# Kernel tuning notes

Measured on AMD Instinct MI355X. Metric: run time of the kernel, lower is better.

The kernel has to match this reference:

```python
import jax, jax.numpy as jnp
import numpy as np

N = 100000
E = 1600000
IN_FEATS = 128
H_FEATS = 128
NUM_CLASSES = 64
BN_EPS = 1e-5


def setup_inputs() -> dict:
    key = jax.random.key(0)
    ks = jax.random.split(key, 16)
    inp = {
        "in_feat": jax.random.normal(ks[0], (N, IN_FEATS), dtype=jnp.float32),
        "src": jax.random.randint(ks[1], (E,), 0, N, dtype=jnp.int64),
        "dst": jax.random.randint(ks[2], (E,), 0, N, dtype=jnp.int64),
        # GraphConv weights (glorot-ish scale) and biases
        "W0": jax.random.normal(ks[3], (IN_FEATS, H_FEATS), dtype=jnp.float32) / np.sqrt(IN_FEATS),
        "b0": jnp.zeros((H_FEATS,), dtype=jnp.float32),
        "W1": jax.random.normal(ks[4], (H_FEATS, H_FEATS), dtype=jnp.float32) / np.sqrt(H_FEATS),
        "b1": jnp.zeros((H_FEATS,), dtype=jnp.float32),
        "W2": jax.random.normal(ks[5], (H_FEATS, NUM_CLASSES), dtype=jnp.float32) / np.sqrt(H_FEATS),
        "b2": jnp.zeros((NUM_CLASSES,), dtype=jnp.float32),
        # BatchNorm affine params
        "gamma0": jnp.ones((H_FEATS,), dtype=jnp.float32),
        "beta0": jnp.zeros((H_FEATS,), dtype=jnp.float32),
        "gamma1": jnp.ones((H_FEATS,), dtype=jnp.float32),
        "beta1": jnp.zeros((H_FEATS,), dtype=jnp.float32),
    }
    return inp


def _graph_conv(src, dst, h, W, b):
    # DGL GraphConv, norm='both': D_dst^{-1/2} A (D_src^{-1/2} h W) + b
    ones = jnp.ones((src.shape[0],), dtype=h.dtype)
    deg_out = jnp.clip(jax.ops.segment_sum(ones, src, num_segments=N), 1.0)
    deg_in = jnp.clip(jax.ops.segment_sum(ones, dst, num_segments=N), 1.0)
    h = h * jax.lax.rsqrt(deg_out)[:, None]
    h = h @ W  # mult weight before aggregation (same math either way)
    agg = jax.ops.segment_sum(h[src], dst, num_segments=N)  # SpMM
    return agg * jax.lax.rsqrt(deg_in)[:, None] + b


def _batch_norm(h, gamma, beta):
    # BatchNorm1d in training mode: biased batch stats over the node axis
    mean = jnp.mean(h, axis=0)
    var = jnp.mean(jnp.square(h - mean), axis=0)
    return (h - mean) * jax.lax.rsqrt(var + BN_EPS) * gamma + beta


def reference(in_feat, src, dst, W0, b0, W1, b1, W2, b2, gamma0, beta0, gamma1, beta1):
    h = _graph_conv(src, dst, in_feat, W0, b0)
    h = jax.nn.relu(_batch_norm(h, gamma0, beta0))  # dropout p=0 -> identity
    h = _graph_conv(src, dst, h, W1, b1)
    h = jax.nn.relu(_batch_norm(h, gamma1, beta1))
    return _graph_conv(src, dst, h, W2, b2)
```

## Files before the change

kernel.cpp:

```cpp
#include <hip/hip_runtime.h>

#define NFEAT 128
#define BT 2048
#define BSH 9
#define BSZ 512
#define NP 256

typedef __attribute__((ext_vector_type(8))) short short8v;
typedef __attribute__((ext_vector_type(4))) float float4v;

static inline size_t align_up(size_t x, size_t a) { return (x + a - 1) & ~(a - 1); }

__device__ inline unsigned short f2bf(float f) {
  unsigned u = __float_as_uint(f);
  u += 0x7FFF + ((u >> 16) & 1);
  return (unsigned short)(u >> 16);
}
__device__ inline unsigned pack2bf(float lo, float hi) {
  return ((unsigned)f2bf(lo)) | (((unsigned)f2bf(hi)) << 16);
}
__device__ inline float bflo(unsigned u) { return __uint_as_float(u << 16); }
__device__ inline float bfhi(unsigned u) { return __uint_as_float(u & 0xFFFF0000u); }

__global__ __launch_bounds__(256) void k_bcount(const int* __restrict__ src,
                                                const int* __restrict__ dst,
                                                int* __restrict__ cnt, int E, int nb, int NBK) {
  __shared__ int hD[256], hS[256];
  const int t = threadIdx.x, b = blockIdx.x;
  hD[t] = 0; hS[t] = 0;
  __syncthreads();
  const int e0 = b * BT, e1 = min(E, e0 + BT);
  for (int e = e0 + t; e < e1; e += 256) {
    atomicAdd(&hD[dst[e] >> BSH], 1);
    atomicAdd(&hS[src[e] >> BSH], 1);
  }
  __syncthreads();
  if (t < NBK) {
    cnt[t * nb + b] = hD[t];
    cnt[(NBK + t) * nb + b] = hS[t];
  }
}

__global__ __launch_bounds__(512) void k_scanA(const int* __restrict__ in,
                                               int* __restrict__ out,
                                               int* __restrict__ bsum, int n) {
  __shared__ int tmp[512];
  const int t = threadIdx.x;
  const int i = blockIdx.x * 512 + t;
  int v = (i < n) ? in[i] : 0;
  tmp[t] = v;
  __syncthreads();
  for (int off = 1; off < 512; off <<= 1) {
    int y = (t >= off) ? tmp[t - off] : 0;
    __syncthreads();
    tmp[t] += y;
    __syncthreads();
  }
  int incl = tmp[t];
  if (i < n) out[i] = incl - v;
  if (t == 511) bsum[blockIdx.x] = incl;
}

__global__ __launch_bounds__(1024) void k_scanB(const int* __restrict__ bsum,
                                                int* __restrict__ bscan, int nb1) {
  __shared__ int tmp[1024];
  const int t = threadIdx.x;
  int v = (t < nb1) ? bsum[t] : 0;
  tmp[t] = v;
  __syncthreads();
  for (int off = 1; off < 1024; off <<= 1) {
    int y = (t >= off) ? tmp[t - off] : 0;
    __syncthreads();
    tmp[t] += y;
    __syncthreads();
  }
  bscan[t] = tmp[t] - v;
}

__global__ __launch_bounds__(512) void k_scanC(int* __restrict__ out,
                                               const int* __restrict__ bscan, int n) {
  const int i = blockIdx.x * 512 + threadIdx.x;
  if (i < n) out[i] += bscan[blockIdx.x];
}

__global__ __launch_bounds__(256) void k_bplace(const int* __restrict__ src,
                                                const int* __restrict__ dst,
                                                const int* __restrict__ off,
                                                int* __restrict__ buf, int E, int nb, int NBK) {
  __shared__ int cD[256], cS[256];
  const int t = threadIdx.x, b = blockIdx.x;
  if (t < NBK) {
    cD[t] = off[t * nb + b];
    cS[t] = off[(NBK + t) * nb + b];
  }
  __syncthreads();
  const int e0 = b * BT, e1 = min(E, e0 + BT);
  for (int e = e0 + t; e < e1; e += 256) {
    int s = src[e];
    int d = dst[e];
    int pD = atomicAdd(&cD[d >> BSH], 1);
    buf[pD] = ((d & (BSZ - 1)) << 17) | s;
    int pS = atomicAdd(&cS[s >> BSH], 1);
    buf[pS] = s;
  }
}

__global__ __launch_bounds__(256) void k_bcsr(const int* __restrict__ buf,
                                              const int* __restrict__ off,
                                              int* __restrict__ row_ptr,
                                              float* __restrict__ rsq_in,
                                              int* __restrict__ col,
                                              int E, int nb, int NBK, int N) {
  const int k = blockIdx.x, t = threadIdx.x;
  const int lo = off[k * nb];
  const int hi = (k + 1 < NBK) ? off[(k + 1) * nb] : E;
  __shared__ int cnt[BSZ];
  __shared__ int sc[BSZ];
  __shared__ int part[64];
  cnt[t] = 0; cnt[t + 256] = 0;
  __syncthreads();
  for (int e = lo + t; e < hi; e += 256) atomicAdd(&cnt[((unsigned)buf[e]) >> 17], 1);
  __syncthreads();
  if (t < 64) {
    int r = 0;
#pragma unroll
    for (int j = 0; j < 8; ++j) r += cnt[t * 8 + j];
    part[t] = r;
  }
  __syncthreads();
  if (t == 0) {
    int run = 0;
    for (int i = 0; i < 64; ++i) { int v = part[i]; part[i] = run; run += v; }
  }
  __syncthreads();
  if (t < 64) {
    int run = part[t];
#pragma unroll
    for (int j = 0; j < 8; ++j) { int v = cnt[t * 8 + j]; sc[t * 8 + j] = run; run += v; }
  }
  __syncthreads();
  for (int idx = t; idx < BSZ; idx += 256) {
    int n = (k << BSH) + idx;
    if (n < N) {
      row_ptr[n] = lo + sc[idx];
      int c = cnt[idx]; if (c < 1) c = 1;
      rsq_in[n] = 1.0f / sqrtf((float)c);
    }
    cnt[idx] = sc[idx];
  }
  if (k == NBK - 1 && t == 0) row_ptr[N] = E;
  __syncthreads();
  for (int e = lo + t; e < hi; e += 256) {
    int w = buf[e];
    int p = atomicAdd(&cnt[((unsigned)w) >> 17], 1);
    col[lo + p] = w & 0x1FFFF;
  }
}

__global__ __launch_bounds__(256) void k_bdeg(const int* __restrict__ buf,
                                              const int* __restrict__ off,
                                              float* __restrict__ rsq_out,
                                              int E, int nb, int NBK, int N) {
  const int k = blockIdx.x, t = threadIdx.x;
  const int lo = off[(NBK + k) * nb];
  const int hi = (k + 1 < NBK) ? off[(NBK + k + 1) * nb] : 2 * E;
  __shared__ int cnt[BSZ];
  cnt[t] = 0; cnt[t + 256] = 0;
  __syncthreads();
  for (int e = lo + t; e < hi; e += 256) atomicAdd(&cnt[buf[e] & (BSZ - 1)], 1);
  __syncthreads();
  for (int idx = t; idx < BSZ; idx += 256) {
    int n = (k << BSH) + idx;
    if (n < N) {
      int c = cnt[idx]; if (c < 1) c = 1;
      rsq_out[n] = 1.0f / sqrtf((float)c);
    }
  }
}

__global__ __launch_bounds__(256) void k_wprep(const float* __restrict__ W0,
                                               const float* __restrict__ W1,
                                               const float* __restrict__ W2,
                                               unsigned short* __restrict__ Wt0,
                                               unsigned short* __restrict__ Wt1,
                                               unsigned short* __restrict__ Wt2) {
  int t = blockIdx.x * 256 + threadIdx.x;
  if (t < 16384) {
    int c = t >> 7, k = t & 127;
    Wt0[c * 128 + k] = f2bf(W0[k * 128 + c]);
  } else if (t < 32768) {
    int u = t - 16384;
    int c = u >> 7, k = u & 127;
    Wt1[c * 128 + k] = f2bf(W1[k * 128 + c]);
  } else if (t < 40960) {
    int u = t - 32768;
    int c = u >> 7, k = u & 127;
    Wt2[c * 128 + k] = f2bf(W2[k * 64 + c]);
  }
}

template <int CC>
__global__ __launch_bounds__(256) void k_gemm_mfma(
    const float* __restrict__ X32, const unsigned short* __restrict__ Xbf,
    const unsigned short* __restrict__ Wt,
    unsigned short* __restrict__ Ybf, const float* __restrict__ rsq_out,
    const float* __restrict__ bnscale, const float* __restrict__ bnshift,
    int Nrows, int mode) {
  constexpr int XBYTES = 64 * 256;
  constexpr int WBYTES = CC * 256;
  __shared__ __align__(16) char lds[XBYTES + WBYTES];
  const int tid = threadIdx.x;
  const int rowBase = blockIdx.x * 64;

  for (int u = tid; u < CC * 16; u += 256) {
    int c = u >> 4, kq = u & 15;
    uint4 v = *(const uint4*)(Wt + c * 128 + kq * 8);
    int byte = (c * 256 + kq * 16) ^ ((c & 7) << 4);
    *(uint4*)(&lds[XBYTES + byte]) = v;
  }
  if (mode == 0) {
#pragma unroll
    for (int i = 0; i < 8; ++i) {
      int u = tid + i * 256;
      int r = u >> 5, kq = u & 31;
      int gr = rowBase + r;
      float4 v = make_float4(0.f, 0.f, 0.f, 0.f);
      if (gr < Nrows) v = *(const float4*)(X32 + (size_t)gr * 128 + kq * 4);
      ushort4 o;
      o.x = f2bf(v.x); o.y = f2bf(v.y); o.z = f2bf(v.z); o.w = f2bf(v.w);
      int byte = (r * 256 + kq * 8) ^ ((r & 7) << 4);
      *(ushort4*)(&lds[byte]) = o;
    }
  } else {
#pragma unroll
    for (int i = 0; i < 4; ++i) {
      int u = tid + i * 256;
      int r = u >> 4, kq = u & 15;
      int gr = rowBase + r;
      uint4 v = make_uint4(0, 0, 0, 0);
      if (gr < Nrows) v = *(const uint4*)(Xbf + (size_t)gr * 128 + kq * 8);
      float f0 = bflo(v.x), f1 = bfhi(v.x), f2 = bflo(v.y), f3 = bfhi(v.y);
      float f4 = bflo(v.z), f5 = bfhi(v.z), f6 = bflo(v.w), f7 = bfhi(v.w);
      const float4 sA = *(const float4*)(bnscale + kq * 8);
      const float4 sB = *(const float4*)(bnscale + kq * 8 + 4);
      const float4 hA = *(const float4*)(bnshift + kq * 8);
      const float4 hB = *(const float4*)(bnshift + kq * 8 + 4);
      f0 = fmaxf(f0 * sA.x + hA.x, 0.f); f1 = fmaxf(f1 * sA.y + hA.y, 0.f);
      f2 = fmaxf(f2 * sA.z + hA.z, 0.f); f3 = fmaxf(f3 * sA.w + hA.w, 0.f);
      f4 = fmaxf(f4 * sB.x + hB.x, 0.f); f5 = fmaxf(f5 * sB.y + hB.y, 0.f);
      f6 = fmaxf(f6 * sB.z + hB.z, 0.f); f7 = fmaxf(f7 * sB.w + hB.w, 0.f);
      uint4 o;
      o.x = pack2bf(f0, f1); o.y = pack2bf(f2, f3);
      o.z = pack2bf(f4, f5); o.w = pack2bf(f6, f7);
      int byte = (r * 256 + kq * 16) ^ ((r & 7) << 4);
      *(uint4*)(&lds[byte]) = o;
    }
  }
  __syncthreads();

  const int wv = tid >> 6;
  const int l = tid & 63;
  const int l16 = l & 15, lk = l >> 4;

  short8v a[4];
  const int arow = wv * 16 + l16;
#pragma unroll
  for (int kk = 0; kk < 4; ++kk) {
    int byte = (arow * 256 + kk * 64 + lk * 16) ^ ((arow & 7) << 4);
    a[kk] = *(const short8v*)(&lds[byte]);
  }

  float4v acc[CC / 16];
#pragma unroll
  for (int ct = 0; ct < CC / 16; ++ct) acc[ct] = (float4v){0.f, 0.f, 0.f, 0.f};

#pragma unroll
  for (int ct = 0; ct < CC / 16; ++ct) {
    const int col = ct * 16 + l16;
#pragma unroll
    for (int kk = 0; kk < 4; ++kk) {
      int byte = XBYTES + ((col * 256 + kk * 64 + lk * 16) ^ ((col & 7) << 4));
      short8v b = *(const short8v*)(&lds[byte]);
      acc[ct] = __builtin_amdgcn_mfma_f32_16x16x32_bf16(a[kk], b, acc[ct], 0, 0, 0);
    }
  }

  const int row0 = rowBase + wv * 16 + lk * 4;
  float scr[4];
#pragma unroll
  for (int r = 0; r < 4; ++r) scr[r] = (row0 + r < Nrows) ? rsq_out[row0 + r] : 0.f;
#pragma unroll
  for (int ct = 0; ct < CC / 16; ++ct) {
#pragma unroll
    for (int r = 0; r < 4; ++r) {
      int row = row0 + r;
      if (row < Nrows)
        Ybf[(size_t)row * CC + ct * 16 + l16] = f2bf(acc[ct][r] * scr[r]);
    }
  }
}

template <int F, int OUT_BF>
__global__ __launch_bounds__(256) void k_spmm2(const int* __restrict__ row_ptr,
                                               const int* __restrict__ colidx,
                                               const unsigned short* __restrict__ xW,
                                               void* __restrict__ outv,
                                               const float* __restrict__ rsq_in,
                                               const float* __restrict__ bias, int Nrows) {
  constexpr int FL = F / 8;
  constexpr int G = 64 / FL;
  const int node = blockIdx.x * 4 + (threadIdx.x >> 6);
  if (node >= Nrows) return;
  const int l = threadIdx.x & 63;
  const int fl = l % FL, g = l / FL;
  const int e0 = row_ptr[node];
  const int e1 = row_ptr[node + 1];
  float acc[8] = {};
  int e = e0 + g;
  for (; e + G < e1; e += 2 * G) {
    int s0 = colidx[e];
    int s1 = colidx[e + G];
    uint4 v0 = *(const uint4*)&xW[(size_t)s0 * F + fl * 8];
    uint4 v1 = *(const uint4*)&xW[(size_t)s1 * F + fl * 8];
    acc[0] += bflo(v0.x); acc[1] += bfhi(v0.x); acc[2] += bflo(v0.y); acc[3] += bfhi(v0.y);
    acc[4] += bflo(v0.z); acc[5] += bfhi(v0.z); acc[6] += bflo(v0.w); acc[7] += bfhi(v0.w);
    acc[0] += bflo(v1.x); acc[1] += bfhi(v1.x); acc[2] += bflo(v1.y); acc[3] += bfhi(v1.y);
    acc[4] += bflo(v1.z); acc[5] += bfhi(v1.z); acc[6] += bflo(v1.w); acc[7] += bfhi(v1.w);
  }
  if (e < e1) {
    int s0 = colidx[e];
    uint4 v0 = *(const uint4*)&xW[(size_t)s0 * F + fl * 8];
    acc[0] += bflo(v0.x); acc[1] += bfhi(v0.x); acc[2] += bflo(v0.y); acc[3] += bfhi(v0.y);
    acc[4] += bflo(v0.z); acc[5] += bfhi(v0.z); acc[6] += bflo(v0.w); acc[7] += bfhi(v0.w);
  }
#pragma unroll
  for (int m = FL; m < 64; m <<= 1) {
#pragma unroll
    for (int j = 0; j < 8; ++j) acc[j] += __shfl_xor(acc[j], m);
  }
  if (g != 0) return;
  const float sc = rsq_in[node];
  const float4 bA = *(const float4*)&bias[fl * 8];
  const float4 bB = *(const float4*)&bias[fl * 8 + 4];
  float o0 = acc[0] * sc + bA.x, o1 = acc[1] * sc + bA.y;
  float o2 = acc[2] * sc + bA.z, o3 = acc[3] * sc + bA.w;
  float o4 = acc[4] * sc + bB.x, o5 = acc[5] * sc + bB.y;
  float o6 = acc[6] * sc + bB.z, o7 = acc[7] * sc + bB.w;
  if (OUT_BF) {
    uint4 w;
    w.x = pack2bf(o0, o1); w.y = pack2bf(o2, o3);
    w.z = pack2bf(o4, o5); w.w = pack2bf(o6, o7);
    *(uint4*)&((unsigned short*)outv)[(size_t)node * F + fl * 8] = w;
  } else {
    float* out = (float*)outv;
    *(float4*)&out[(size_t)node * F + fl * 8] = make_float4(o0, o1, o2, o3);
    *(float4*)&out[(size_t)node * F + fl * 8 + 4] = make_float4(o4, o5, o6, o7);
  }
}

__global__ __launch_bounds__(256) void k_bn_stats_bf(const unsigned short* __restrict__ h,
                                                     float* __restrict__ psum,
                                                     float* __restrict__ pssq, int Nrows) {
  const int t = threadIdx.x;
  const int fs = t & 15;
  const int rg = t >> 4;
  float s[8] = {}, ss[8] = {};
  for (int r = blockIdx.x * 16 + rg; r < Nrows; r += gridDim.x * 16) {
    uint4 v = *(const uint4*)&h[(size_t)r * 128 + fs * 8];
    float f0 = bflo(v.x), f1 = bfhi(v.x), f2 = bflo(v.y), f3 = bfhi(v.y);
    float f4 = bflo(v.z), f5 = bfhi(v.z), f6 = bflo(v.w), f7 = bfhi(v.w);
    s[0] += f0; ss[0] += f0 * f0; s[1] += f1; ss[1] += f1 * f1;
    s[2] += f2; ss[2] += f2 * f2; s[3] += f3; ss[3] += f3 * f3;
    s[4] += f4; ss[4] += f4 * f4; s[5] += f5; ss[5] += f5 * f5;
    s[6] += f6; ss[6] += f6 * f6; s[7] += f7; ss[7] += f7 * f7;
  }
#pragma unroll
  for (int m = 16; m < 64; m <<= 1) {
#pragma unroll
    for (int j = 0; j < 8; ++j) { s[j] += __shfl_xor(s[j], m); ss[j] += __shfl_xor(ss[j], m); }
  }
  __shared__ float lsum[4][128], lssq[4][128];
  const int wv = t >> 6, wl = t & 63;
  if (wl < 16) {
#pragma unroll
    for (int j = 0; j < 8; ++j) { lsum[wv][wl * 8 + j] = s[j]; lssq[wv][wl * 8 + j] = ss[j]; }
  }
  __syncthreads();
  if (t < 128) {
    psum[(size_t)blockIdx.x * 128 + t] = lsum[0][t] + lsum[1][t] + lsum[2][t] + lsum[3][t];
    pssq[(size_t)blockIdx.x * 128 + t] = lssq[0][t] + lssq[1][t] + lssq[2][t] + lssq[3][t];
  }
}

__global__ __launch_bounds__(256) void k_bn_final(const float* __restrict__ psum,
                                                  const float* __restrict__ pssq,
                                                  const float* __restrict__ gamma,
                                                  const float* __restrict__ beta,
                                                  float* __restrict__ scale,
                                                  float* __restrict__ shift, int Nrows) {
  const int t = threadIdx.x;
  const int f = t & 127, half = t >> 7;
  float s = 0.f, ss = 0.f;
  for (int b = half * (NP / 2); b < (half + 1) * (NP / 2); ++b) {
    s += psum[(size_t)b * 128 + f];
    ss += pssq[(size_t)b * 128 + f];
  }
  __shared__ float ls[2][128], lss[2][128];
  ls[half][f] = s; lss[half][f] = ss;
  __syncthreads();
  if (t < 128) {
    float sum = ls[0][t] + ls[1][t];
    float sumsq = lss[0][t] + lss[1][t];
    float inv_n = 1.0f / (float)Nrows;
    float mean = sum * inv_n;
    float var = sumsq * inv_n - mean * mean;
    if (var < 0.f) var = 0.f;
    float sc = gamma[t] * (1.0f / sqrtf(var + 1e-5f));
    scale[t] = sc;
    shift[t] = beta[t] - mean * sc;
  }
}

extern "C" void kernel_launch(void* const* d_in, const int* in_sizes, int n_in,
                              void* d_out, int out_size, void* d_ws, size_t ws_size,
                              hipStream_t stream) {
  const float* in_feat = (const float*)d_in[0];
  const int* src = (const int*)d_in[1];
  const int* dst = (const int*)d_in[2];
  const float* W0 = (const float*)d_in[3];
  const float* b0 = (const float*)d_in[4];
  const float* W1 = (const float*)d_in[5];
  const float* b1 = (const float*)d_in[6];
  const float* W2 = (const float*)d_in[7];
  const float* b2 = (const float*)d_in[8];
  const float* gamma0 = (const float*)d_in[9];
  const float* beta0 = (const float*)d_in[10];
  const float* gamma1 = (const float*)d_in[11];
  const float* beta1 = (const float*)d_in[12];
  float* out = (float*)d_out;

  const int N = in_sizes[0] / NFEAT;
  const int E = in_sizes[1];

  const int nb = (E + BT - 1) / BT;
  const int NBK = (N + BSZ - 1) / BSZ;
  const int L = 2 * NBK * nb;
  const int nb1 = (L + 511) / 512;

  char* p = (char*)d_ws;
  auto carve = [&](size_t bytes) {
    char* q = p;
    p += align_up(bytes, 256);
    return q;
  };
  int* cnt = (int*)carve((size_t)L * 4);
  int* off = (int*)carve((size_t)L * 4);
  int* bsum = (int*)carve(1024 * 4);
  int* bscan = (int*)carve(1024 * 4);
  int* row_ptr = (int*)carve((size_t)(N + 1) * 4);
  int* col = (int*)carve((size_t)E * 4);
  float* rsq_out = (float*)carve((size_t)N * 4);
  float* rsq_in = (float*)carve((size_t)N * 4);
  float* psum0 = (float*)carve((size_t)NP * 128 * 4);
  float* pssq0 = (float*)carve((size_t)NP * 128 * 4);
  float* psum1 = (float*)carve((size_t)NP * 128 * 4);
  float* pssq1 = (float*)carve((size_t)NP * 128 * 4);
  float* bn_scale0 = (float*)carve(128 * 4);
  float* bn_shift0 = (float*)carve(128 * 4);
  float* bn_scale1 = (float*)carve(128 * 4);
  float* bn_shift1 = (float*)carve(128 * 4);
  unsigned short* Wt0 = (unsigned short*)carve(16384 * 2);
  unsigned short* Wt1 = (unsigned short*)carve(16384 * 2);
  unsigned short* Wt2 = (unsigned short*)carve(8192 * 2);
  unsigned short* xWbf = (unsigned short*)carve((size_t)N * NFEAT * 2);
  unsigned short* hbf = (unsigned short*)carve((size_t)N * NFEAT * 2);
  int* buf = (int*)carve((size_t)2 * E * 4);

  k_wprep<<<160, 256, 0, stream>>>(W0, W1, W2, Wt0, Wt1, Wt2);
  k_bcount<<<nb, 256, 0, stream>>>(src, dst, cnt, E, nb, NBK);
  k_scanA<<<nb1, 512, 0, stream>>>(cnt, off, bsum, L);
  k_scanB<<<1, 1024, 0, stream>>>(bsum, bscan, nb1);
  k_scanC<<<nb1, 512, 0, stream>>>(off, bscan, L);
  k_bplace<<<nb, 256, 0, stream>>>(src, dst, off, buf, E, nb, NBK);
  k_bcsr<<<NBK, 256, 0, stream>>>(buf, off, row_ptr, rsq_in, col, E, nb, NBK, N);
  k_bdeg<<<NBK, 256, 0, stream>>>(buf, off, rsq_out, E, nb, NBK, N);

  const int GR = (N + 63) / 64;
  const int GS = (N + 3) / 4;

  k_gemm_mfma<128><<<GR, 256, 0, stream>>>(in_feat, nullptr, Wt0, xWbf, rsq_out,
                                           nullptr, nullptr, N, 0);
  k_spmm2<128, 1><<<GS, 256, 0, stream>>>(row_ptr, col, xWbf, hbf, rsq_in, b0, N);
  k_bn_stats_bf<<<NP, 256, 0, stream>>>(hbf, psum0, pssq0, N);
  k_bn_final<<<1, 256, 0, stream>>>(psum0, pssq0, gamma0, beta0, bn_scale0, bn_shift0, N);

  k_gemm_mfma<128><<<GR, 256, 0, stream>>>(nullptr, hbf, Wt1, xWbf, rsq_out,
                                           bn_scale0, bn_shift0, N, 1);
  k_spmm2<128, 1><<<GS, 256, 0, stream>>>(row_ptr, col, xWbf, hbf, rsq_in, b1, N);
  k_bn_stats_bf<<<NP, 256, 0, stream>>>(hbf, psum1, pssq1, N);
  k_bn_final<<<1, 256, 0, stream>>>(psum1, pssq1, gamma1, beta1, bn_scale1, bn_shift1, N);

  k_gemm_mfma<64><<<GR, 256, 0, stream>>>(nullptr, hbf, Wt2, xWbf, rsq_out,
                                          bn_scale1, bn_shift1, N, 1);
  k_spmm2<64, 0><<<GS, 256, 0, stream>>>(row_ptr, col, xWbf, out, rsq_in, b2, N);
}
```

Before: 517.7 us.

## Fold scan fixup into consumers, merge CSR and degree kernels, unroll SpMM gather

```diff
diff --git a/kernel.cpp b/kernel.cpp
--- a/kernel.cpp
+++ b/kernel.cpp
@@ -21,6 +21,9 @@
 }
 __device__ inline float bflo(unsigned u) { return __uint_as_float(u << 16); }
 __device__ inline float bfhi(unsigned u) { return __uint_as_float(u & 0xFFFF0000u); }
+__device__ inline int goff(const int* __restrict__ off, const int* __restrict__ bscan, int i) {
+  return off[i] + bscan[i >> 9];
+}
 
 __global__ __launch_bounds__(256) void k_bcount(const int* __restrict__ src,
                                                 const int* __restrict__ dst,
@@ -77,21 +80,16 @@
   bscan[t] = tmp[t] - v;
 }
 
-__global__ __launch_bounds__(512) void k_scanC(int* __restrict__ out,
-                                               const int* __restrict__ bscan, int n) {
-  const int i = blockIdx.x * 512 + threadIdx.x;
-  if (i < n) out[i] += bscan[blockIdx.x];
-}
-
 __global__ __launch_bounds__(256) void k_bplace(const int* __restrict__ src,
                                                 const int* __restrict__ dst,
                                                 const int* __restrict__ off,
+                                                const int* __restrict__ bscan,
                                                 int* __restrict__ buf, int E, int nb, int NBK) {
   __shared__ int cD[256], cS[256];
   const int t = threadIdx.x, b = blockIdx.x;
   if (t < NBK) {
-    cD[t] = off[t * nb + b];
-    cS[t] = off[(NBK + t) * nb + b];
+    cD[t] = goff(off, bscan, t * nb + b);
+    cS[t] = goff(off, bscan, (NBK + t) * nb + b);
   }
   __syncthreads();
   const int e0 = b * BT, e1 = min(E, e0 + BT);
@@ -105,18 +103,20 @@
   }
 }
 
-__global__ __launch_bounds__(256) void k_bcsr(const int* __restrict__ buf,
-                                              const int* __restrict__ off,
-                                              int* __restrict__ row_ptr,
-                                              float* __restrict__ rsq_in,
-                                              int* __restrict__ col,
-                                              int E, int nb, int NBK, int N) {
+__global__ __launch_bounds__(256) void k_bcsr_deg(const int* __restrict__ buf,
+                                                  const int* __restrict__ off,
+                                                  const int* __restrict__ bscan,
+                                                  int* __restrict__ row_ptr,
+                                                  float* __restrict__ rsq_in,
+                                                  float* __restrict__ rsq_out,
+                                                  int* __restrict__ col,
+                                                  int E, int nb, int NBK, int N) {
   const int k = blockIdx.x, t = threadIdx.x;
-  const int lo = off[k * nb];
-  const int hi = (k + 1 < NBK) ? off[(k + 1) * nb] : E;
   __shared__ int cnt[BSZ];
   __shared__ int sc[BSZ];
   __shared__ int part[64];
+  const int lo = goff(off, bscan, k * nb);
+  const int hi = (k + 1 < NBK) ? goff(off, bscan, (k + 1) * nb) : E;
   cnt[t] = 0; cnt[t + 256] = 0;
   __syncthreads();
   for (int e = lo + t; e < hi; e += 256) atomicAdd(&cnt[((unsigned)buf[e]) >> 17], 1);
@@ -155,19 +155,12 @@
     int p = atomicAdd(&cnt[((unsigned)w) >> 17], 1);
     col[lo + p] = w & 0x1FFFF;
   }
-}
-
-__global__ __launch_bounds__(256) void k_bdeg(const int* __restrict__ buf,
-                                              const int* __restrict__ off,
-                                              float* __restrict__ rsq_out,
-                                              int E, int nb, int NBK, int N) {
-  const int k = blockIdx.x, t = threadIdx.x;
-  const int lo = off[(NBK + k) * nb];
-  const int hi = (k + 1 < NBK) ? off[(NBK + k + 1) * nb] : 2 * E;
-  __shared__ int cnt[BSZ];
+  __syncthreads();
   cnt[t] = 0; cnt[t + 256] = 0;
   __syncthreads();
-  for (int e = lo + t; e < hi; e += 256) atomicAdd(&cnt[buf[e] & (BSZ - 1)], 1);
+  const int lo2 = goff(off, bscan, (NBK + k) * nb);
+  const int hi2 = (k + 1 < NBK) ? goff(off, bscan, (NBK + k + 1) * nb) : 2 * E;
+  for (int e = lo2 + t; e < hi2; e += 256) atomicAdd(&cnt[buf[e] & (BSZ - 1)], 1);
   __syncthreads();
   for (int idx = t; idx < BSZ; idx += 256) {
     int n = (k << BSH) + idx;
@@ -317,17 +310,25 @@
   const int e1 = row_ptr[node + 1];
   float acc[8] = {};
   int e = e0 + g;
-  for (; e + G < e1; e += 2 * G) {
+  for (; e + 3 * G < e1; e += 4 * G) {
     int s0 = colidx[e];
     int s1 = colidx[e + G];
+    int s2 = colidx[e + 2 * G];
+    int s3 = colidx[e + 3 * G];
     uint4 v0 = *(const uint4*)&xW[(size_t)s0 * F + fl * 8];
     uint4 v1 = *(const uint4*)&xW[(size_t)s1 * F + fl * 8];
+    uint4 v2 = *(const uint4*)&xW[(size_t)s2 * F + fl * 8];
+    uint4 v3 = *(const uint4*)&xW[(size_t)s3 * F + fl * 8];
     acc[0] += bflo(v0.x); acc[1] += bfhi(v0.x); acc[2] += bflo(v0.y); acc[3] += bfhi(v0.y);
     acc[4] += bflo(v0.z); acc[5] += bfhi(v0.z); acc[6] += bflo(v0.w); acc[7] += bfhi(v0.w);
     acc[0] += bflo(v1.x); acc[1] += bfhi(v1.x); acc[2] += bflo(v1.y); acc[3] += bfhi(v1.y);
     acc[4] += bflo(v1.z); acc[5] += bfhi(v1.z); acc[6] += bflo(v1.w); acc[7] += bfhi(v1.w);
-  }
-  if (e < e1) {
+    acc[0] += bflo(v2.x); acc[1] += bfhi(v2.x); acc[2] += bflo(v2.y); acc[3] += bfhi(v2.y);
+    acc[4] += bflo(v2.z); acc[5] += bfhi(v2.z); acc[6] += bflo(v2.w); acc[7] += bfhi(v2.w);
+    acc[0] += bflo(v3.x); acc[1] += bfhi(v3.x); acc[2] += bflo(v3.y); acc[3] += bfhi(v3.y);
+    acc[4] += bflo(v3.z); acc[5] += bfhi(v3.z); acc[6] += bflo(v3.w); acc[7] += bfhi(v3.w);
+  }
+  for (; e < e1; e += G) {
     int s0 = colidx[e];
     uint4 v0 = *(const uint4*)&xW[(size_t)s0 * F + fl * 8];
     acc[0] += bflo(v0.x); acc[1] += bfhi(v0.x); acc[2] += bflo(v0.y); acc[3] += bfhi(v0.y);
@@ -480,10 +481,9 @@
   k_bcount<<<nb, 256, 0, stream>>>(src, dst, cnt, E, nb, NBK);
   k_scanA<<<nb1, 512, 0, stream>>>(cnt, off, bsum, L);
   k_scanB<<<1, 1024, 0, stream>>>(bsum, bscan, nb1);
-  k_scanC<<<nb1, 512, 0, stream>>>(off, bscan, L);
-  k_bplace<<<nb, 256, 0, stream>>>(src, dst, off, buf, E, nb, NBK);
-  k_bcsr<<<NBK, 256, 0, stream>>>(buf, off, row_ptr, rsq_in, col, E, nb, NBK, N);
-  k_bdeg<<<NBK, 256, 0, stream>>>(buf, off, rsq_out, E, nb, NBK, N);
+  k_bplace<<<nb, 256, 0, stream>>>(src, dst, off, bscan, buf, E, nb, NBK);
+  k_bcsr_deg<<<NBK, 256, 0, stream>>>(buf, off, bscan, row_ptr, rsq_in, rsq_out, col,
+                                      E, nb, NBK, N);
 
   const int GR = (N + 63) / 64;
   const int GS = (N + 3) / 4;
```

After: 518.8 us. No clear change (+0.2%).
